# Performance work log

Measured on AMD Instinct MI355X. Metric: run time of the kernel, lower is better.

Reference implementation:

```python
import jax, jax.numpy as jnp
import numpy as np

EPS = float(np.finfo(np.float32).eps)

# (joint_id, joint_name, parent_name) in the module's fkm_computation_order
ORDER = [
    (1, 'rHip', 'hip'), (2, 'rKnee', 'rHip'), (3, 'rAnkle', 'rKnee'), (4, 'rToe', 'rAnkle'),
    (6, 'lHip', 'hip'), (7, 'lKnee', 'lHip'), (8, 'lAnkle', 'lKnee'), (9, 'lToe', 'lAnkle'),
    (11, 'spine', 'hip'), (12, 'spine1', 'spine'), (13, 'thorax', 'spine1'), (14, 'neck', 'thorax'),
    (15, 'head', 'neck'), (16, 'lShoulderAnchor', 'spine1'), (17, 'lShoulder', 'lShoulderAnchor'),
    (18, 'lElbow', 'lShoulder'), (19, 'lWrist', 'lElbow'), (20, 'lThumb', 'lWrist'),
    (22, 'lWristEnd', 'lWrist'), (24, 'rShoulderAnchor', 'spine1'), (25, 'rShoulder', 'rShoulderAnchor'),
    (26, 'rElbow', 'rShoulder'), (27, 'rWrist', 'rElbow'), (28, 'rThumb', 'rWrist'),
    (30, 'rWristEnd', 'rWrist'),
]


def axis_angle_to_matrix(a):
    """Rodrigues formula, batched. a: [B,3] -> [B,3,3]."""
    theta = jnp.linalg.norm(a, axis=-1, keepdims=True)  # [B,1]
    r = a / (theta + EPS)                               # [B,3]
    r0, r1, r2 = r[:, 0], r[:, 1], r[:, 2]
    z = jnp.zeros_like(r0)
    # skew-symmetric S with S[0,1]=-r2, S[0,2]=r1, S[1,2]=-r0 (as in torch code)
    S = jnp.stack([
        jnp.stack([z, -r2, r1], axis=-1),
        jnp.stack([r2, z, -r0], axis=-1),
        jnp.stack([-r1, r0, z], axis=-1),
    ], axis=-2)  # [B,3,3]
    th = theta[..., None]  # [B,1,1]
    I = jnp.eye(3, dtype=a.dtype)
    return I + jnp.sin(th) * S + (1.0 - jnp.cos(th)) * (S @ S)


def setup_inputs() -> dict:
    key = jax.random.key(0)
    k1, k2 = jax.random.split(key)
    B = 262144
    x = jax.random.normal(k1, (B, 99), dtype=jnp.float32)
    offset = jax.random.normal(k2, (32, 3), dtype=jnp.float32)
    return {"x": x, "offset": offset}


def reference(x, offset):
    # hip root: position from first 3 dims, orientation from dims 3:6
    pos = {"hip": offset[0] + x[:, 0:3]}                # [B,3]
    ang = {"hip": axis_angle_to_matrix(x[:, 3:6])}      # [B,3,3]
    # local rotations for every joint in the chain: dims [3*id+3 : 3*id+6]
    local = {name: axis_angle_to_matrix(x[:, 3 * i + 3: 3 * i + 6]) for i, name, _ in ORDER}
    # sequential forward kinematics down the tree
    for i, cur, par in ORDER:
        # offset[i] @ R_parent  (row-vector times matrix), then translate
        pos[cur] = jnp.einsum('j,bjk->bk', offset[i], ang[par]) + pos[par]
        ang[cur] = local[cur] @ ang[par]
    # positions in the same order as get_joint_positions(): hip then chain order
    return jnp.stack([pos['hip']] + [pos[c] for _, c, _ in ORDER], axis=1)  # [B,26,3]
```

## Files before the change

### kernel.cpp

```cpp
#include <hip/hip_runtime.h>

#define TPB  128
#define RPW  64
#define XDIM 99
#define NJ   26
#define OUTW 78

constexpr int OFF_IDX[NJ] = {0,1,2,3,4,6,7,8,9,11,12,13,14,15,16,17,18,19,20,22,24,25,26,27,28,30};
constexpr int PAR[NJ]     = {-1,0,1,2,3,0,5,6,7,0,9,10,11,12,10,14,15,16,17,17,10,20,21,22,23,23};

__device__ __forceinline__ float fast_rcp(float a)  { return __builtin_amdgcn_rcpf(a); }
__device__ __forceinline__ float fast_sqrt(float a) { return __builtin_amdgcn_sqrtf(a); }

__device__ __forceinline__ void rodrigues(float ax, float ay, float az, float* R) {
    const float EPS = 1.1920928955078125e-07f;
    float t = fast_sqrt(ax*ax + ay*ay + az*az);
    float inv = fast_rcp(t + EPS);
    float r0 = ax*inv, r1 = ay*inv, r2 = az*inv;
    float s, c;
    __sincosf(t, &s, &c);
    float omc = 1.0f - c;
    float r00 = r0*r0, r11 = r1*r1, r22 = r2*r2;
    float r01 = r0*r1, r02 = r0*r2, r12 = r1*r2;
    R[0] = 1.0f - omc*(r11 + r22);
    R[1] = -s*r2 + omc*r01;
    R[2] =  s*r1 + omc*r02;
    R[3] =  s*r2 + omc*r01;
    R[4] = 1.0f - omc*(r00 + r22);
    R[5] = -s*r0 + omc*r12;
    R[6] = -s*r1 + omc*r02;
    R[7] =  s*r0 + omc*r12;
    R[8] = 1.0f - omc*(r00 + r11);
}

#define STEP(s) do {                                                          \
    const int i_  = OFF_IDX[(s)];                                             \
    const int pa_ = PAR[(s)];                                                 \
    float L[9];                                                               \
    rodrigues(row[3*i_+3], row[3*i_+4], row[3*i_+5], L);                      \
    const float o0 = off[3*i_], o1 = off[3*i_+1], o2 = off[3*i_+2];           \
    _Pragma("unroll")                                                         \
    for (int c = 0; c < 3; ++c)                                               \
        pp[(s)][c] = o0*ang[pa_][c] + o1*ang[pa_][3+c] + o2*ang[pa_][6+c]     \
                   + pp[pa_][c];                                              \
    _Pragma("unroll")                                                         \
    for (int j = 0; j < 3; ++j)                                               \
        _Pragma("unroll")                                                     \
        for (int kk = 0; kk < 3; ++kk)                                        \
            ang[(s)][3*j+kk] = L[3*j+0]*ang[pa_][0+kk]                        \
                             + L[3*j+1]*ang[pa_][3+kk]                        \
                             + L[3*j+2]*ang[pa_][6+kk];                       \
} while (0)

__global__ __launch_bounds__(TPB, 3) void skel_fk(const float* __restrict__ x,
                                                  const float* __restrict__ off,
                                                  float* __restrict__ out) {
    __shared__ __align__(16) float buf[RPW * XDIM];
    const int t = threadIdx.x;
    const int w = t >> 6;
    const int l = t & 63;
    const int row0 = blockIdx.x * RPW;
    const float* gsrc = x + (long long)row0 * XDIM;

    if (w == 0) {
        #pragma unroll
        for (int j = 0; j < 12; ++j)
            __builtin_amdgcn_global_load_lds(
                (const __attribute__((address_space(1))) unsigned int*)(gsrc + 256*j + 4*l),
                (__attribute__((address_space(3))) unsigned int*)(buf + 256*j),
                16, 0, 0);
        __builtin_amdgcn_global_load_lds(
            (const __attribute__((address_space(1))) unsigned int*)(gsrc + 6144 + l),
            (__attribute__((address_space(3))) unsigned int*)(buf + 6144),
            4, 0, 0);
    } else {
        #pragma unroll
        for (int j = 12; j < 24; ++j)
            __builtin_amdgcn_global_load_lds(
                (const __attribute__((address_space(1))) unsigned int*)(gsrc + 256*j + 4*l),
                (__attribute__((address_space(3))) unsigned int*)(buf + 256*j),
                16, 0, 0);
        #pragma unroll
        for (int kk = 1; kk < 3; ++kk)
            __builtin_amdgcn_global_load_lds(
                (const __attribute__((address_space(1))) unsigned int*)(gsrc + 6144 + 64*kk + l),
                (__attribute__((address_space(3))) unsigned int*)(buf + 6144 + 64*kk),
                4, 0, 0);
    }
    __syncthreads();

    const float* row = &buf[l * XDIM];
    float ang[NJ][9];
    float pp[NJ][3];

    {
        float R[9];
        rodrigues(row[3], row[4], row[5], R);
        #pragma unroll
        for (int q = 0; q < 9; ++q) ang[0][q] = R[q];
        pp[0][0] = off[0] + row[0];
        pp[0][1] = off[1] + row[1];
        pp[0][2] = off[2] + row[2];
    }

    if (w == 0) {
        #pragma unroll
        for (int s = 1; s <= 13; ++s) STEP(s);
    } else {
        STEP(9);
        STEP(10);
        #pragma unroll
        for (int s = 14; s < NJ; ++s) STEP(s);
    }
    __syncthreads();

    {
        float2* p2 = reinterpret_cast<float2*>(buf);
        if (w == 0) {
            float2* wr2 = p2 + 39 * l;
            #pragma unroll
            for (int j = 0; j < 21; ++j) {
                float2 v;
                v.x = pp[(2*j)   / 3][(2*j)   % 3];
                v.y = pp[(2*j+1) / 3][(2*j+1) % 3];
                wr2[j] = v;
            }
        } else {
            float2* wr2 = p2 + 39 * l + 21;
            #pragma unroll
            for (int j = 0; j < 18; ++j) {
                const int f = 42 + 2*j;
                float2 v;
                v.x = pp[f / 3][f % 3];
                v.y = pp[(f+1) / 3][(f+1) % 3];
                wr2[j] = v;
            }
        }
    }
    __syncthreads();

    {
        float4* ob4 = reinterpret_cast<float4*>(out + (long long)row0 * OUTW);
        const float4* b4 = reinterpret_cast<const float4*>(buf);
        #pragma unroll
        for (int j = 0; j < 9; ++j)
            ob4[t + 128*j] = b4[t + 128*j];
        if (t < 96) ob4[1152 + t] = b4[1152 + t];
    }
}

extern "C" void kernel_launch(void* const* d_in, const int* in_sizes, int n_in,
                              void* d_out, int out_size, void* d_ws, size_t ws_size,
                              hipStream_t stream) {
    const float* x   = (const float*)d_in[0];
    const float* off = (const float*)d_in[1];
    float* out = (float*)d_out;
    const int B = in_sizes[0] / XDIM;
    const int grid = B / RPW;
    skel_fk<<<grid, TPB, 0, stream>>>(x, off, out);
}
```

Measured before the change: 37.76 us.

## Split skeleton FK tree across four wavefronts per 64-row block

Doubles the block to 256 threads so each of four wavefronts handles one branch of the kinematic tree (right leg, left leg, spine/head, and each arm). The global-to-LDS load and the output store are redistributed over four waves. This shortens the serial dependency chain per thread and lowers register pressure, in exchange for recomputing the shared spine prefix (steps 9 and 10) in two waves and writing scalar instead of float2 values to LDS.

```diff
diff --git a/kernel.cpp b/kernel.cpp
--- a/kernel.cpp
+++ b/kernel.cpp
@@ -1,6 +1,6 @@
 #include <hip/hip_runtime.h>
 
-#define TPB  128
+#define TPB  256
 #define RPW  64
 #define XDIM 99
 #define NJ   26
@@ -52,7 +52,7 @@
                              + L[3*j+2]*ang[pa_][6+kk];                       \
 } while (0)
 
-__global__ __launch_bounds__(TPB, 3) void skel_fk(const float* __restrict__ x,
+__global__ __launch_bounds__(TPB, 4) void skel_fk(const float* __restrict__ x,
                                                   const float* __restrict__ off,
                                                   float* __restrict__ out) {
     __shared__ __align__(16) float buf[RPW * XDIM];
@@ -62,30 +62,20 @@
     const int row0 = blockIdx.x * RPW;
     const float* gsrc = x + (long long)row0 * XDIM;
 
-    if (w == 0) {
-        #pragma unroll
-        for (int j = 0; j < 12; ++j)
-            __builtin_amdgcn_global_load_lds(
-                (const __attribute__((address_space(1))) unsigned int*)(gsrc + 256*j + 4*l),
-                (__attribute__((address_space(3))) unsigned int*)(buf + 256*j),
-                16, 0, 0);
+    #pragma unroll
+    for (int j = 0; j < 6; ++j) {
+        const int jj = 6 * w + j;
         __builtin_amdgcn_global_load_lds(
-            (const __attribute__((address_space(1))) unsigned int*)(gsrc + 6144 + l),
-            (__attribute__((address_space(3))) unsigned int*)(buf + 6144),
+            (const __attribute__((address_space(1))) unsigned int*)(gsrc + 256*jj + 4*l),
+            (__attribute__((address_space(3))) unsigned int*)(buf + 256*jj),
+            16, 0, 0);
+    }
+    if (w >= 1) {
+        const int kk = w - 1;
+        __builtin_amdgcn_global_load_lds(
+            (const __attribute__((address_space(1))) unsigned int*)(gsrc + 6144 + 64*kk + l),
+            (__attribute__((address_space(3))) unsigned int*)(buf + 6144 + 64*kk),
             4, 0, 0);
-    } else {
-        #pragma unroll
-        for (int j = 12; j < 24; ++j)
-            __builtin_amdgcn_global_load_lds(
-                (const __attribute__((address_space(1))) unsigned int*)(gsrc + 256*j + 4*l),
-                (__attribute__((address_space(3))) unsigned int*)(buf + 256*j),
-                16, 0, 0);
-        #pragma unroll
-        for (int kk = 1; kk < 3; ++kk)
-            __builtin_amdgcn_global_load_lds(
-                (const __attribute__((address_space(1))) unsigned int*)(gsrc + 6144 + 64*kk + l),
-                (__attribute__((address_space(3))) unsigned int*)(buf + 6144 + 64*kk),
-                4, 0, 0);
     }
     __syncthreads();
 
@@ -105,35 +95,43 @@
 
     if (w == 0) {
         #pragma unroll
-        for (int s = 1; s <= 13; ++s) STEP(s);
+        for (int s = 1; s <= 8; ++s) STEP(s);
+    } else if (w == 1) {
+        #pragma unroll
+        for (int s = 9; s <= 13; ++s) STEP(s);
+    } else if (w == 2) {
+        STEP(9); STEP(10);
+        #pragma unroll
+        for (int s = 14; s <= 19; ++s) STEP(s);
     } else {
-        STEP(9);
-        STEP(10);
+        STEP(9); STEP(10);
         #pragma unroll
-        for (int s = 14; s < NJ; ++s) STEP(s);
+        for (int s = 20; s <= 25; ++s) STEP(s);
     }
     __syncthreads();
 
     {
-        float2* p2 = reinterpret_cast<float2*>(buf);
+        float* srow = &buf[l * OUTW];
         if (w == 0) {
-            float2* wr2 = p2 + 39 * l;
             #pragma unroll
-            for (int j = 0; j < 21; ++j) {
-                float2 v;
-                v.x = pp[(2*j)   / 3][(2*j)   % 3];
-                v.y = pp[(2*j+1) / 3][(2*j+1) % 3];
-                wr2[j] = v;
+            for (int s = 1; s <= 8; ++s) {
+                srow[3*s+0] = pp[s][0]; srow[3*s+1] = pp[s][1]; srow[3*s+2] = pp[s][2];
+            }
+        } else if (w == 1) {
+            srow[0] = pp[0][0]; srow[1] = pp[0][1]; srow[2] = pp[0][2];
+            #pragma unroll
+            for (int s = 9; s <= 13; ++s) {
+                srow[3*s+0] = pp[s][0]; srow[3*s+1] = pp[s][1]; srow[3*s+2] = pp[s][2];
+            }
+        } else if (w == 2) {
+            #pragma unroll
+            for (int s = 14; s <= 19; ++s) {
+                srow[3*s+0] = pp[s][0]; srow[3*s+1] = pp[s][1]; srow[3*s+2] = pp[s][2];
             }
         } else {
-            float2* wr2 = p2 + 39 * l + 21;
             #pragma unroll
-            for (int j = 0; j < 18; ++j) {
-                const int f = 42 + 2*j;
-                float2 v;
-                v.x = pp[f / 3][f % 3];
-                v.y = pp[(f+1) / 3][(f+1) % 3];
-                wr2[j] = v;
+            for (int s = 20; s <= 25; ++s) {
+                srow[3*s+0] = pp[s][0]; srow[3*s+1] = pp[s][1]; srow[3*s+2] = pp[s][2];
             }
         }
     }
@@ -143,9 +141,9 @@
         float4* ob4 = reinterpret_cast<float4*>(out + (long long)row0 * OUTW);
         const float4* b4 = reinterpret_cast<const float4*>(buf);
         #pragma unroll
-        for (int j = 0; j < 9; ++j)
-            ob4[t + 128*j] = b4[t + 128*j];
-        if (t < 96) ob4[1152 + t] = b4[1152 + t];
+        for (int j = 0; j < 4; ++j)
+            ob4[t + 256*j] = b4[t + 256*j];
+        if (t < 224) ob4[1024 + t] = b4[1024 + t];
     }
 }
 
```

New measurement: 36.77 us. 1.03x faster.
